# Kernel optimization log

Hardware: AMD Instinct MI355X
Metric: run time of the kernel (lower is better)

The kernel has to match this reference:

```python
import jax, jax.numpy as jnp
import numpy as np
from jax import lax

NUM_BLOCK_X, NUM_BLOCK_Y = 6, 6
NUM_BLOCKS = NUM_BLOCK_X * NUM_BLOCK_Y  # 36


def build_grid_adjacency(nx_, ny_):
    # Mirrors PathFinder128Net.build_grid_adjacency exactly (same edge order).
    src, dst = [], []
    for i in range(nx_):
        for j in range(ny_):
            for dx, dy in [(-1, 0), (0, -1), (0, 1), (1, 0)]:
                x, y = i + dx, j + dy
                if 0 <= x < nx_ and 0 <= y < ny_:
                    src.append(j * nx_ + i)   # block_coord_to_block_id(i, j)
                    dst.append(y * nx_ + x)   # block_coord_to_block_id(x, y)
    return np.asarray(src, np.int32), np.asarray(dst, np.int32)


def setup_inputs() -> dict:
    key = jax.random.key(0)
    ks = jax.random.split(key, 12)
    B = 64
    x = jax.random.normal(ks[0], (B, 1, 128, 128), jnp.float32)
    W = 0.05  # conv init scale
    F = 0.02  # fc init scale
    src, dst = build_grid_adjacency(NUM_BLOCK_X, NUM_BLOCK_Y)  # 120 edges
    n_edges = src.shape[0]
    return {
        "x": x,
        "w1": jax.random.normal(ks[1], (32, 1, 5, 5), jnp.float32) * W,
        "b1": jnp.zeros((32,), jnp.float32),
        "w2": jax.random.normal(ks[2], (32, 32, 5, 5), jnp.float32) * W,
        "b2": jnp.zeros((32,), jnp.float32),
        "w3": jax.random.normal(ks[3], (64, 32, 5, 5), jnp.float32) * W,
        "b3": jnp.zeros((64,), jnp.float32),
        "w4": jax.random.normal(ks[4], (64, 64, 5, 5), jnp.float32) * W,
        "b4": jnp.zeros((64,), jnp.float32),
        "w_ed1": jax.random.normal(ks[5], (1600, 256), jnp.float32) * F,
        "b_ed1": jnp.zeros((256,), jnp.float32),
        "w_ed2": jax.random.normal(ks[6], (256, n_edges), jnp.float32) * F,
        "b_ed2": jnp.zeros((n_edges,), jnp.float32),
        "w_ep1": jax.random.normal(ks[7], (1600, 256), jnp.float32) * F,
        "b_ep1": jnp.zeros((256,), jnp.float32),
        "w_ep2": jax.random.normal(ks[8], (256, NUM_BLOCKS), jnp.float32) * F,
        "b_ep2": jnp.zeros((NUM_BLOCKS,), jnp.float32),
        "edge_src": jnp.asarray(src),
        "edge_dst": jnp.asarray(dst),
    }


def _conv(h, w, b):
    # torch Conv2d, kernel 5, stride 1, no padding, NO activation in between
    h = lax.conv_general_dilated(h, w, (1, 1), "VALID",
                                 dimension_numbers=("NCHW", "OIHW", "NCHW"))
    return h + b[None, :, None, None]


def _pool4(h):
    return lax.reduce_window(h, -jnp.inf, lax.max, (1, 1, 4, 4), (1, 1, 4, 4), "VALID")


def reference(x, w1, b1, w2, b2, w3, b3, w4, b4,
              w_ed1, b_ed1, w_ed2, b_ed2, w_ep1, b_ep1, w_ep2, b_ep2,
              edge_src, edge_dst):
    B = x.shape[0]
    h = _pool4(_conv(_conv(x, w1, b1), w2, b2))          # [B,32,30,30]
    h = _pool4(_conv(_conv(h, w3, b3), w4, b4))          # [B,64,5,5]
    emb = h.reshape(B, -1)                               # [B,1600]

    # edge / endpoint heads: Linear -> ReLU -> Linear -> Sigmoid
    E = jax.nn.sigmoid(jax.nn.relu(emb @ w_ed1 + b_ed1) @ w_ed2 + b_ed2)  # [B,120]
    P = jax.nn.sigmoid(jax.nn.relu(emb @ w_ep1 + b_ep1) @ w_ep2 + b_ep2)  # [B,36]

    # build_paths_recursive with DAMP provenance: symbols are (src,dst) 2-tuples.
    # extend_path maps ((a,b),(b,c)) -> (b,c), i.e. new symbols are already the
    # existing edge set, so the fixpoint terminates after the first iteration
    # (len(merged.symbols) == len(old.symbols)) and is_endpoint is applied to the
    # ORIGINAL connected distribution. A path symbol (u,v) survives is_endpoint
    # conjoined with endpoint evidence at both ends (DAMP conj = product):
    final = E * P[:, edge_src] * P[:, edge_dst]          # [B,120]

    # paths.get_probabilities()[:, 0] -> probability of the first symbol, which
    # is adjacency[0] = (0, 6) for the 6x6 grid.
    return final[:, 0]
```

## Files before the change

kernel.cpp:

```cpp
#include <hip/hip_runtime.h>
#include <math.h>

typedef __attribute__((ext_vector_type(8))) short bf16x8;
typedef __attribute__((ext_vector_type(4))) float f32x4;
typedef unsigned short ushort_t;

#define WS_W12   0
#define WS_B12   2592
#define WS_WMF   2624
#define WS_B34   (2624 + 165888)
#define WS_WMF12 (WS_B34 + 64)
#define WS_P1    (WS_WMF12 + 2560)
#define WS_EMB   (WS_P1 + 64*30*30*32)
#define WS_LOG   (WS_EMB + 102400)
#define WS_WPART WS_P1
#define WS_BPART (WS_P1 + 8*165888)

#define PLST 1880

__device__ __forceinline__ unsigned short f2bf(float f) {
    unsigned u = __float_as_uint(f);
    u += 0x7FFF + ((u >> 16) & 1);
    return (unsigned short)(u >> 16);
}

__global__ __launch_bounds__(128) void k_prep12(
    const float* __restrict__ w1, const float* __restrict__ b1,
    const float* __restrict__ w2, const float* __restrict__ b2,
    float* __restrict__ W12, float* __restrict__ B12)
{
    __shared__ float sW2[800];
    __shared__ float sW1[800];
    int oc = blockIdx.x;
    int t  = threadIdx.x;
    for (int i = t; i < 800; i += 128) {
        sW2[i] = w2[oc * 800 + i];
        sW1[i] = w1[i];
    }
    __syncthreads();
    if (t < 81) {
        int u = t / 9, v = t % 9;
        float acc[4] = {0.f, 0.f, 0.f, 0.f};
        #pragma unroll
        for (int e = 0; e < 25; ++e) {
            int ey = e / 5, ex = e % 5;
            int du = u - ey, dv = v - ex;
            if ((unsigned)du <= 4u && (unsigned)dv <= 4u) {
                int ep = du * 5 + dv;
                for (int mc = 0; mc < 32; ++mc)
                    acc[e & 3] = fmaf(sW2[mc * 25 + e], sW1[mc * 25 + ep],
                                      acc[e & 3]);
            }
        }
        W12[t * 32 + oc] = (acc[0] + acc[1]) + (acc[2] + acc[3]);
    }
    if (t < 32) {
        float ws = 0.f;
        #pragma unroll
        for (int e = 0; e < 25; ++e) ws += sW2[t * 25 + e];
        float p = b1[t] * ws;
        #pragma unroll
        for (int off = 16; off; off >>= 1) p += __shfl_down(p, off, 64);
        if (t == 0) B12[oc] = p + b2[oc];
    }
}

__global__ __launch_bounds__(256) void k_prep34p(
    const float* __restrict__ w3, const float* __restrict__ b3,
    const float* __restrict__ w4,
    float* __restrict__ Wpart, float* __restrict__ Bpart)
{
    __shared__ float sW3c[800];
    int icg = blockIdx.x >> 3;
    int mcc = blockIdx.x & 7;
    int t   = threadIdx.x;
    int oc  = t & 63;
    int icl = t >> 6;
    int ic  = icg * 4 + icl;

    for (int i = t; i < 800; i += 256) {
        int mcl = i / 100, r = i % 100;
        sW3c[i] = w3[(mcc * 8 + mcl) * 800 + icg * 100 + r];
    }
    __syncthreads();

    float acc[81];
    #pragma unroll
    for (int u = 0; u < 81; ++u) acc[u] = 0.f;
    float bacc = 0.f;

    for (int mcl = 0; mcl < 8; ++mcl) {
        int mc = mcc * 8 + mcl;
        float w4r[25];
        #pragma unroll
        for (int e = 0; e < 25; ++e) w4r[e] = w4[oc * 1600 + mc * 25 + e];
        const float* w3r = &sW3c[(mcl * 4 + icl) * 25];
        #pragma unroll
        for (int e2 = 0; e2 < 25; ++e2) {
            int ey = e2 / 5, ex = e2 % 5;
            #pragma unroll
            for (int e1 = 0; e1 < 25; ++e1) {
                int u = (ey + e1 / 5) * 9 + (ex + e1 % 5);
                acc[u] = fmaf(w4r[e2], w3r[e1], acc[u]);
            }
        }
        if (icl == 0) {
            float ws = 0.f;
            #pragma unroll
            for (int e = 0; e < 25; ++e) ws += w4r[e];
            bacc = fmaf(b3[mc], ws, bacc);
        }
    }

    for (int uv = 0; uv < 81; ++uv)
        Wpart[((mcc * 32 + ic) * 81 + uv) * 64 + oc] = acc[uv];
    if (icl == 0) Bpart[mcc * 64 + oc] = bacc;
}

__global__ __launch_bounds__(256) void k_prep34s(
    const float* __restrict__ Wpart, const float* __restrict__ Bpart,
    const float* __restrict__ b4, const float* __restrict__ W12,
    ushort_t* __restrict__ Wmf, float* __restrict__ B34,
    ushort_t* __restrict__ Wmf12)
{
    int bid = blockIdx.x;
    int t   = threadIdx.x;
    int i   = bid * 256 + t;
    if (i < 165888) {
        float s = 0.f;
        #pragma unroll
        for (int c = 0; c < 8; ++c) s += Wpart[c * 165888 + i];
        int oc = i & 63, r = i >> 6;
        int ic = r / 81, uv = r % 81;
        int idx = (uv * 16 + (oc >> 4) * 4 + (ic >> 3)) * 128
                + (oc & 15) * 8 + (ic & 7);
        Wmf[idx] = f2bf(s);
    }
    if (bid == 648 && t < 64) {
        int oc = t;
        float s = b4[oc];
        #pragma unroll
        for (int c = 0; c < 8; ++c) s += Bpart[c * 64 + oc];
        B34[oc] = s;
    }
    if (bid >= 649) {
        int i2 = (bid - 649) * 256 + t;
        int e   = i2 & 7;
        int n   = (i2 >> 3) & 15;
        int kc  = (i2 >> 7) & 3;
        int so  = i2 >> 9;
        int s   = so >> 1, och = so & 1;
        int ky  = 2 * s + (kc >> 1);
        int kx  = 8 * (kc & 1) + e;
        float v = (ky <= 8 && kx <= 8) ? W12[(ky * 9 + kx) * 32 + och * 16 + n]
                                       : 0.f;
        Wmf12[i2] = f2bf(v);
    }
}

__global__ __launch_bounds__(256) void k_conv12m(
    const float* __restrict__ x, const ushort_t* __restrict__ Wmf12,
    const float* __restrict__ B12, ushort_t* __restrict__ P1bf)
{
    __shared__ ushort_t sX[8 * PLST];

    int b  = blockIdx.x / 30;
    int py = blockIdx.x % 30;
    int t  = threadIdx.x;

    if (t < 221) {
        int rowL = t / 17, qg = t % 17;
        int absrow = 4 * py + rowL;
        if (absrow > 127) absrow = 127;
        const float* xr = x + (b * 128 + absrow) * 128;
        int c0 = qg * 8;
        float fs[16];
        #pragma unroll
        for (int q4 = 0; q4 < 4; ++q4) {
            int c = c0 + 4 * q4;
            float4 f;
            if (c <= 124) f = *(const float4*)(xr + c);
            else { f.x = 0.f; f.y = 0.f; f.z = 0.f; f.w = 0.f; }
            fs[4 * q4 + 0] = f.x; fs[4 * q4 + 1] = f.y;
            fs[4 * q4 + 2] = f.z; fs[4 * q4 + 3] = f.w;
        }
        unsigned d[8];
        #pragma unroll
        for (int j = 0; j < 8; ++j)
            d[j] = (unsigned)f2bf(fs[2 * j]) |
                   ((unsigned)f2bf(fs[2 * j + 1]) << 16);
        int eoff = rowL * 144 + c0;
        #pragma unroll
        for (int p = 0; p < 8; ++p) {
            uint4 wv;
            int k = p >> 1;
            if ((p & 1) == 0) {
                wv.x = d[k]; wv.y = d[k + 1]; wv.z = d[k + 2]; wv.w = d[k + 3];
            } else {
                wv.x = (d[k] >> 16)     | (d[k + 1] << 16);
                wv.y = (d[k + 1] >> 16) | (d[k + 2] << 16);
                wv.z = (d[k + 2] >> 16) | (d[k + 3] << 16);
                wv.w = (d[k + 3] >> 16) | (d[k + 4] << 16);
            }
            *(uint4*)(sX + p * PLST + eoff) = wv;
        }
    }

    int l   = t & 63;
    int wv_ = t >> 6;
    int m16 = l & 15;
    int kc  = l >> 4;

    bf16x8 Bf[5][2];
    {
        const ushort_t* wb = Wmf12 + kc * 128 + m16 * 8;
        #pragma unroll
        for (int s = 0; s < 5; ++s)
            #pragma unroll
            for (int och = 0; och < 2; ++och)
                Bf[s][och] = *(const bf16x8*)(wb + (s * 2 + och) * 512);
    }
    float bias0 = B12[m16];
    float bias1 = B12[16 + m16];
    __syncthreads();

    int baseC = (m16 & 7) * PLST + (kc >> 1) * 144
              + 8 * (m16 >> 3) + 8 * (kc & 1);

    #pragma unroll
    for (int xi = 0; xi < 2; ++xi) {
        int xt = wv_ * 2 + xi;
        const ushort_t* ap = sX + baseC + xt * 16;
        float pm0 = -INFINITY, pm1 = -INFINITY;
        #pragma unroll
        for (int y = 0; y < 4; ++y) {
            f32x4 a0 = {0.f, 0.f, 0.f, 0.f}, a1 = a0;
            #pragma unroll
            for (int s = 0; s < 5; ++s) {
                bf16x8 av = *(const bf16x8*)(ap + (y + 2 * s) * 144);
                a0 = __builtin_amdgcn_mfma_f32_16x16x32_bf16(av, Bf[s][0], a0, 0, 0, 0);
                a1 = __builtin_amdgcn_mfma_f32_16x16x32_bf16(av, Bf[s][1], a1, 0, 0, 0);
            }
            pm0 = fmaxf(pm0, fmaxf(fmaxf(a0[0], a0[1]), fmaxf(a0[2], a0[3])));
            pm1 = fmaxf(pm1, fmaxf(fmaxf(a1[0], a1[1]), fmaxf(a1[2], a1[3])));
        }
        int px = xt * 4 + (l >> 4);
        if (px < 30) {
            int ob = ((b * 30 + py) * 30 + px) * 32 + m16;
            P1bf[ob]      = f2bf(pm0 + bias0);
            P1bf[ob + 16] = f2bf(pm1 + bias1);
        }
    }
}

__global__ __launch_bounds__(320) void k_conv34m(
    const ushort_t* __restrict__ P1bf, const ushort_t* __restrict__ Wmf,
    const float* __restrict__ B34, float* __restrict__ emb)
{
    __shared__ ushort_t sA[28 * 960];

    int b  = blockIdx.x >> 2;
    int nt = blockIdx.x & 3;
    int t  = threadIdx.x;

    const uint4* gsrc = (const uint4*)(P1bf + b * 28800);
    for (int i = t; i < 3360; i += 320)
        ((uint4*)sA)[i] = gsrc[i];
    __syncthreads();

    int w  = t >> 6;
    int l  = t & 63;
    int m16 = l & 15;
    int kc  = l >> 4;
    int iy = m16 >> 2, ix = m16 & 3;

    int baseU = (w * 4 + iy) * 960 + ix * 32 + kc * 8;

    f32x4 acc0 = {0.f,0.f,0.f,0.f}, acc1 = acc0, acc2 = acc0,
          acc3 = acc0, acc4 = acc0;

    const ushort_t* wp = Wmf + (nt * 4 + kc) * 128 + m16 * 8;

    bf16x8 bcur = *(const bf16x8*)wp;
    int tap = 0;
    for (int ky = 0; ky < 9; ++ky) {
        int rowU = baseU + ky * 960;
        #pragma unroll
        for (int kx = 0; kx < 9; ++kx) {
            bf16x8 bnext = *(const bf16x8*)(wp + (tap + 1) * 2048);
            const ushort_t* ap = sA + rowU + kx * 32;
            bf16x8 a0 = *(const bf16x8*)(ap);
            bf16x8 a1 = *(const bf16x8*)(ap + 128);
            bf16x8 a2 = *(const bf16x8*)(ap + 256);
            bf16x8 a3 = *(const bf16x8*)(ap + 384);
            bf16x8 a4 = *(const bf16x8*)(ap + 512);
            acc0 = __builtin_amdgcn_mfma_f32_16x16x32_bf16(a0, bcur, acc0, 0, 0, 0);
            acc1 = __builtin_amdgcn_mfma_f32_16x16x32_bf16(a1, bcur, acc1, 0, 0, 0);
            acc2 = __builtin_amdgcn_mfma_f32_16x16x32_bf16(a2, bcur, acc2, 0, 0, 0);
            acc3 = __builtin_amdgcn_mfma_f32_16x16x32_bf16(a3, bcur, acc3, 0, 0, 0);
            acc4 = __builtin_amdgcn_mfma_f32_16x16x32_bf16(a4, bcur, acc4, 0, 0, 0);
            bcur = bnext;
            ++tap;
        }
    }

    float bias = B34[nt * 16 + m16];
    #pragma unroll
    for (int q = 0; q < 5; ++q) {
        f32x4 a = (q == 0) ? acc0 : (q == 1) ? acc1 : (q == 2) ? acc2
                : (q == 3) ? acc3 : acc4;
        float mv = fmaxf(fmaxf(a[0], a[1]), fmaxf(a[2], a[3]));
        mv = fmaxf(mv, __shfl_xor(mv, 16, 64));
        mv = fmaxf(mv, __shfl_xor(mv, 32, 64));
        if (l < 16) {
            int oc = nt * 16 + l;
            emb[b * 1600 + oc * 25 + w * 5 + q] = mv + bias;
        }
    }
}

__global__ __launch_bounds__(512) void k_fc(
    const float* __restrict__ emb,
    const float* __restrict__ w_ed1, const float* __restrict__ b_ed1,
    const float* __restrict__ w_ed2, const float* __restrict__ b_ed2,
    const float* __restrict__ w_ep1, const float* __restrict__ b_ep1,
    const float* __restrict__ w_ep2, const float* __restrict__ b_ep2,
    const int* __restrict__ esrc, const int* __restrict__ edst,
    float* __restrict__ logits)
{
    __shared__ float se[1600];
    __shared__ float sh[2][256];
    __shared__ float sred[2][4];

    int head = blockIdx.x >> 6;
    int b    = blockIdx.x & 63;
    int t    = threadIdx.x;
    int j    = t & 255;
    int kh   = t >> 8;

    {
        const float4* src = (const float4*)(emb + b * 1600);
        for (int i = t; i < 400; i += 512) ((float4*)se)[i] = src[i];
    }
    __syncthreads();

    const float* W1 = head ? w_ep1 : w_ed1;
    float a0 = 0.f, a1 = 0.f, a2 = 0.f, a3 = 0.f;
    int k0 = kh * 800;
    #pragma unroll 8
    for (int k = k0; k < k0 + 800; k += 4) {
        a0 = fmaf(se[k + 0], W1[(k + 0) * 256 + j], a0);
        a1 = fmaf(se[k + 1], W1[(k + 1) * 256 + j], a1);
        a2 = fmaf(se[k + 2], W1[(k + 2) * 256 + j], a2);
        a3 = fmaf(se[k + 3], W1[(k + 3) * 256 + j], a3);
    }
    sh[kh][j] = (a0 + a1) + (a2 + a3);
    __syncthreads();

    int c0 = esrc[0], c1 = edst[0];
    if (t < 256) {
        float bias1 = head ? b_ep1[j] : b_ed1[j];
        float h = fmaxf(bias1 + sh[0][j] + sh[1][j], 0.f);
        if (head == 0) {
            float p = h * w_ed2[j * 120];
            #pragma unroll
            for (int off = 32; off; off >>= 1) p += __shfl_down(p, off, 64);
            if ((t & 63) == 0) sred[0][t >> 6] = p;
        } else {
            float p0 = h * w_ep2[j * 36 + c0];
            float p1 = h * w_ep2[j * 36 + c1];
            #pragma unroll
            for (int off = 32; off; off >>= 1) {
                p0 += __shfl_down(p0, off, 64);
                p1 += __shfl_down(p1, off, 64);
            }
            if ((t & 63) == 0) {
                sred[0][t >> 6] = p0;
                sred[1][t >> 6] = p1;
            }
        }
    }
    __syncthreads();
    if (t == 0) {
        float s0 = (sred[0][0] + sred[0][1]) + (sred[0][2] + sred[0][3]);
        if (head == 0) {
            logits[b * 3 + 0] = s0 + b_ed2[0];
        } else {
            float s1 = (sred[1][0] + sred[1][1]) + (sred[1][2] + sred[1][3]);
            logits[b * 3 + 1] = s0 + b_ep2[c0];
            logits[b * 3 + 2] = s1 + b_ep2[c1];
        }
    }
}

__global__ __launch_bounds__(64) void k_final(
    const float* __restrict__ logits, float* __restrict__ out)
{
    int b = threadIdx.x;
    if (b < 64) {
        float e  = logits[b * 3 + 0];
        float p0 = logits[b * 3 + 1];
        float p1 = logits[b * 3 + 2];
        out[b] = (1.f / (1.f + expf(-e))) *
                 (1.f / (1.f + expf(-p0))) *
                 (1.f / (1.f + expf(-p1)));
    }
}

extern "C" void kernel_launch(void* const* d_in, const int* in_sizes, int n_in,
                              void* d_out, int out_size, void* d_ws, size_t ws_size,
                              hipStream_t stream)
{
    const float* x     = (const float*)d_in[0];
    const float* w1    = (const float*)d_in[1];
    const float* b1    = (const float*)d_in[2];
    const float* w2    = (const float*)d_in[3];
    const float* b2    = (const float*)d_in[4];
    const float* w3    = (const float*)d_in[5];
    const float* b3    = (const float*)d_in[6];
    const float* w4    = (const float*)d_in[7];
    const float* b4    = (const float*)d_in[8];
    const float* w_ed1 = (const float*)d_in[9];
    const float* b_ed1 = (const float*)d_in[10];
    const float* w_ed2 = (const float*)d_in[11];
    const float* b_ed2 = (const float*)d_in[12];
    const float* w_ep1 = (const float*)d_in[13];
    const float* b_ep1 = (const float*)d_in[14];
    const float* w_ep2 = (const float*)d_in[15];
    const float* b_ep2 = (const float*)d_in[16];
    const int*   esrc  = (const int*)d_in[17];
    const int*   edst  = (const int*)d_in[18];

    float* ws  = (float*)d_ws;
    float* out = (float*)d_out;

    ushort_t* Wmf   = (ushort_t*)(ws + WS_WMF);
    ushort_t* Wmf12 = (ushort_t*)(ws + WS_WMF12);
    ushort_t* P1bf  = (ushort_t*)(ws + WS_P1);

    k_prep12<<<32, 128, 0, stream>>>(w1, b1, w2, b2, ws + WS_W12, ws + WS_B12);
    k_prep34p<<<64, 256, 0, stream>>>(w3, b3, w4, ws + WS_WPART, ws + WS_BPART);
    k_prep34s<<<669, 256, 0, stream>>>(ws + WS_WPART, ws + WS_BPART, b4,
                                       ws + WS_W12, Wmf, ws + WS_B34, Wmf12);
    k_conv12m<<<64 * 30, 256, 0, stream>>>(x, Wmf12, ws + WS_B12, P1bf);
    k_conv34m<<<256, 320, 0, stream>>>(P1bf, Wmf, ws + WS_B34, ws + WS_EMB);
    k_fc<<<128, 512, 0, stream>>>(ws + WS_EMB, w_ed1, b_ed1, w_ed2, b_ed2,
                                  w_ep1, b_ep1, w_ep2, b_ep2, esrc, edst,
                                  ws + WS_LOG);
    k_final<<<1, 64, 0, stream>>>(ws + WS_LOG, out);
}
```

Before: 88.69 us.

## Merge prep kernels, fuse FC heads with final sigmoid, preload conv tiles into registers

Merges the conv1/2 weight-prep kernel with the conv3/4 partial-prep kernel and writes the packed conv12 MFMA weights directly from shared memory. The FC heads and the final sigmoid product become one kernel that handles two batch rows per block, so each weight load is reused for two samples. Both conv kernels now preload their input rows from LDS into register arrays before the MFMA loops, and launch-bounds occupancy hints are added. This cuts two launches and redundant LDS reads, at the cost of higher register pressure and fewer FC blocks (32) to hide memory latency.

```diff
diff --git a/kernel.cpp b/kernel.cpp
--- a/kernel.cpp
+++ b/kernel.cpp
@@ -5,18 +5,14 @@
 typedef __attribute__((ext_vector_type(4))) float f32x4;
 typedef unsigned short ushort_t;
 
-#define WS_W12   0
 #define WS_B12   2592
 #define WS_WMF   2624
 #define WS_B34   (2624 + 165888)
 #define WS_WMF12 (WS_B34 + 64)
 #define WS_P1    (WS_WMF12 + 2560)
 #define WS_EMB   (WS_P1 + 64*30*30*32)
-#define WS_LOG   (WS_EMB + 102400)
 #define WS_WPART WS_P1
 #define WS_BPART (WS_P1 + 8*165888)
-
-#define PLST 1880
 
 __device__ __forceinline__ unsigned short f2bf(float f) {
     unsigned u = __float_as_uint(f);
@@ -24,108 +20,119 @@
     return (unsigned short)(u >> 16);
 }
 
-__global__ __launch_bounds__(128) void k_prep12(
+__global__ __launch_bounds__(256) void k_prepA(
     const float* __restrict__ w1, const float* __restrict__ b1,
     const float* __restrict__ w2, const float* __restrict__ b2,
-    float* __restrict__ W12, float* __restrict__ B12)
-{
-    __shared__ float sW2[800];
-    __shared__ float sW1[800];
-    int oc = blockIdx.x;
-    int t  = threadIdx.x;
-    for (int i = t; i < 800; i += 128) {
-        sW2[i] = w2[oc * 800 + i];
-        sW1[i] = w1[i];
-    }
-    __syncthreads();
-    if (t < 81) {
-        int u = t / 9, v = t % 9;
-        float acc[4] = {0.f, 0.f, 0.f, 0.f};
-        #pragma unroll
-        for (int e = 0; e < 25; ++e) {
-            int ey = e / 5, ex = e % 5;
-            int du = u - ey, dv = v - ex;
-            if ((unsigned)du <= 4u && (unsigned)dv <= 4u) {
-                int ep = du * 5 + dv;
-                for (int mc = 0; mc < 32; ++mc)
-                    acc[e & 3] = fmaf(sW2[mc * 25 + e], sW1[mc * 25 + ep],
-                                      acc[e & 3]);
-            }
-        }
-        W12[t * 32 + oc] = (acc[0] + acc[1]) + (acc[2] + acc[3]);
-    }
-    if (t < 32) {
-        float ws = 0.f;
-        #pragma unroll
-        for (int e = 0; e < 25; ++e) ws += sW2[t * 25 + e];
-        float p = b1[t] * ws;
-        #pragma unroll
-        for (int off = 16; off; off >>= 1) p += __shfl_down(p, off, 64);
-        if (t == 0) B12[oc] = p + b2[oc];
-    }
-}
-
-__global__ __launch_bounds__(256) void k_prep34p(
     const float* __restrict__ w3, const float* __restrict__ b3,
     const float* __restrict__ w4,
+    float* __restrict__ B12, ushort_t* __restrict__ Wmf12,
     float* __restrict__ Wpart, float* __restrict__ Bpart)
 {
-    __shared__ float sW3c[800];
-    int icg = blockIdx.x >> 3;
-    int mcc = blockIdx.x & 7;
-    int t   = threadIdx.x;
-    int oc  = t & 63;
-    int icl = t >> 6;
-    int ic  = icg * 4 + icl;
-
-    for (int i = t; i < 800; i += 256) {
-        int mcl = i / 100, r = i % 100;
-        sW3c[i] = w3[(mcc * 8 + mcl) * 800 + icg * 100 + r];
-    }
-    __syncthreads();
-
-    float acc[81];
-    #pragma unroll
-    for (int u = 0; u < 81; ++u) acc[u] = 0.f;
-    float bacc = 0.f;
-
-    for (int mcl = 0; mcl < 8; ++mcl) {
-        int mc = mcc * 8 + mcl;
-        float w4r[25];
-        #pragma unroll
-        for (int e = 0; e < 25; ++e) w4r[e] = w4[oc * 1600 + mc * 25 + e];
-        const float* w3r = &sW3c[(mcl * 4 + icl) * 25];
-        #pragma unroll
-        for (int e2 = 0; e2 < 25; ++e2) {
-            int ey = e2 / 5, ex = e2 % 5;
-            #pragma unroll
-            for (int e1 = 0; e1 < 25; ++e1) {
-                int u = (ey + e1 / 5) * 9 + (ex + e1 % 5);
-                acc[u] = fmaf(w4r[e2], w3r[e1], acc[u]);
+    __shared__ float smem[1681];
+    int t = threadIdx.x;
+
+    if (blockIdx.x < 32) {
+        float* sW2  = smem;
+        float* sW1  = smem + 800;
+        float* sW12 = smem + 1600;
+        int oc = blockIdx.x;
+        for (int i = t; i < 800; i += 256) {
+            sW2[i] = w2[oc * 800 + i];
+            sW1[i] = w1[i];
+        }
+        __syncthreads();
+        if (t < 81) {
+            int u = t / 9, v = t % 9;
+            float acc[4] = {0.f, 0.f, 0.f, 0.f};
+            #pragma unroll
+            for (int e = 0; e < 25; ++e) {
+                int ey = e / 5, ex = e % 5;
+                int du = u - ey, dv = v - ex;
+                if ((unsigned)du <= 4u && (unsigned)dv <= 4u) {
+                    int ep = du * 5 + dv;
+                    for (int mc = 0; mc < 32; ++mc)
+                        acc[e & 3] = fmaf(sW2[mc * 25 + e], sW1[mc * 25 + ep],
+                                          acc[e & 3]);
+                }
             }
-        }
-        if (icl == 0) {
+            sW12[t] = (acc[0] + acc[1]) + (acc[2] + acc[3]);
+        }
+        if (t < 32) {
             float ws = 0.f;
             #pragma unroll
-            for (int e = 0; e < 25; ++e) ws += w4r[e];
-            bacc = fmaf(b3[mc], ws, bacc);
-        }
-    }
-
-    for (int uv = 0; uv < 81; ++uv)
-        Wpart[((mcc * 32 + ic) * 81 + uv) * 64 + oc] = acc[uv];
-    if (icl == 0) Bpart[mcc * 64 + oc] = bacc;
+            for (int e = 0; e < 25; ++e) ws += sW2[t * 25 + e];
+            float p = b1[t] * ws;
+            #pragma unroll
+            for (int off = 16; off; off >>= 1) p += __shfl_down(p, off, 64);
+            if (t == 0) B12[oc] = p + b2[oc];
+        }
+        __syncthreads();
+        if (t < 160) {
+            int s  = t >> 5;
+            int kc = (t >> 3) & 3;
+            int e  = t & 7;
+            int ky = 2 * s + (kc >> 1);
+            int kx = 8 * (kc & 1) + e;
+            float v = (ky <= 8 && kx <= 8) ? sW12[ky * 9 + kx] : 0.f;
+            int so = s * 2 + (oc >> 4);
+            int i2 = (so << 9) | (kc << 7) | ((oc & 15) << 3) | e;
+            Wmf12[i2] = f2bf(v);
+        }
+    } else {
+        float* sW3c = smem;
+        int bid = blockIdx.x - 32;
+        int icg = bid >> 3;
+        int mcc = bid & 7;
+        int oc  = t & 63;
+        int icl = t >> 6;
+        int ic  = icg * 4 + icl;
+
+        for (int i = t; i < 800; i += 256) {
+            int mcl = i / 100, r = i % 100;
+            sW3c[i] = w3[(mcc * 8 + mcl) * 800 + icg * 100 + r];
+        }
+        __syncthreads();
+
+        float acc[81];
+        #pragma unroll
+        for (int u = 0; u < 81; ++u) acc[u] = 0.f;
+        float bacc = 0.f;
+
+        for (int mcl = 0; mcl < 8; ++mcl) {
+            int mc = mcc * 8 + mcl;
+            float w4r[25];
+            #pragma unroll
+            for (int e = 0; e < 25; ++e) w4r[e] = w4[oc * 1600 + mc * 25 + e];
+            const float* w3r = &sW3c[(mcl * 4 + icl) * 25];
+            #pragma unroll
+            for (int e2 = 0; e2 < 25; ++e2) {
+                int ey = e2 / 5, ex = e2 % 5;
+                #pragma unroll
+                for (int e1 = 0; e1 < 25; ++e1) {
+                    int u = (ey + e1 / 5) * 9 + (ex + e1 % 5);
+                    acc[u] = fmaf(w4r[e2], w3r[e1], acc[u]);
+                }
+            }
+            if (icl == 0) {
+                float ws = 0.f;
+                #pragma unroll
+                for (int e = 0; e < 25; ++e) ws += w4r[e];
+                bacc = fmaf(b3[mc], ws, bacc);
+            }
+        }
+
+        for (int uv = 0; uv < 81; ++uv)
+            Wpart[((mcc * 32 + ic) * 81 + uv) * 64 + oc] = acc[uv];
+        if (icl == 0) Bpart[mcc * 64 + oc] = bacc;
+    }
 }
 
 __global__ __launch_bounds__(256) void k_prep34s(
     const float* __restrict__ Wpart, const float* __restrict__ Bpart,
-    const float* __restrict__ b4, const float* __restrict__ W12,
-    ushort_t* __restrict__ Wmf, float* __restrict__ B34,
-    ushort_t* __restrict__ Wmf12)
-{
-    int bid = blockIdx.x;
-    int t   = threadIdx.x;
-    int i   = bid * 256 + t;
+    const float* __restrict__ b4,
+    ushort_t* __restrict__ Wmf, float* __restrict__ B34)
+{
+    int i = blockIdx.x * 256 + threadIdx.x;
     if (i < 165888) {
         float s = 0.f;
         #pragma unroll
@@ -136,33 +143,20 @@
                 + (oc & 15) * 8 + (ic & 7);
         Wmf[idx] = f2bf(s);
     }
-    if (bid == 648 && t < 64) {
-        int oc = t;
+    if (blockIdx.x == 648 && threadIdx.x < 64) {
+        int oc = threadIdx.x;
         float s = b4[oc];
         #pragma unroll
         for (int c = 0; c < 8; ++c) s += Bpart[c * 64 + oc];
         B34[oc] = s;
     }
-    if (bid >= 649) {
-        int i2 = (bid - 649) * 256 + t;
-        int e   = i2 & 7;
-        int n   = (i2 >> 3) & 15;
-        int kc  = (i2 >> 7) & 3;
-        int so  = i2 >> 9;
-        int s   = so >> 1, och = so & 1;
-        int ky  = 2 * s + (kc >> 1);
-        int kx  = 8 * (kc & 1) + e;
-        float v = (ky <= 8 && kx <= 8) ? W12[(ky * 9 + kx) * 32 + och * 16 + n]
-                                       : 0.f;
-        Wmf12[i2] = f2bf(v);
-    }
-}
-
-__global__ __launch_bounds__(256) void k_conv12m(
+}
+
+__global__ __launch_bounds__(256, 2) void k_conv12m(
     const float* __restrict__ x, const ushort_t* __restrict__ Wmf12,
     const float* __restrict__ B12, ushort_t* __restrict__ P1bf)
 {
-    __shared__ ushort_t sX[8 * PLST];
+    __shared__ ushort_t sX[8 * 1880];
 
     int b  = blockIdx.x / 30;
     int py = blockIdx.x % 30;
@@ -202,7 +196,7 @@
                 wv.z = (d[k + 2] >> 16) | (d[k + 3] << 16);
                 wv.w = (d[k + 3] >> 16) | (d[k + 4] << 16);
             }
-            *(uint4*)(sX + p * PLST + eoff) = wv;
+            *(uint4*)(sX + p * 1880 + eoff) = wv;
         }
     }
 
@@ -224,22 +218,26 @@
     float bias1 = B12[16 + m16];
     __syncthreads();
 
-    int baseC = (m16 & 7) * PLST + (kc >> 1) * 144
+    int baseC = (m16 & 7) * 1880 + (kc >> 1) * 144
               + 8 * (m16 >> 3) + 8 * (kc & 1);
 
     #pragma unroll
     for (int xi = 0; xi < 2; ++xi) {
         int xt = wv_ * 2 + xi;
         const ushort_t* ap = sX + baseC + xt * 16;
+        bf16x8 T[12];
+        #pragma unroll
+        for (int r = 0; r < 12; ++r)
+            T[r] = *(const bf16x8*)(ap + r * 144);
+
         float pm0 = -INFINITY, pm1 = -INFINITY;
         #pragma unroll
         for (int y = 0; y < 4; ++y) {
             f32x4 a0 = {0.f, 0.f, 0.f, 0.f}, a1 = a0;
             #pragma unroll
             for (int s = 0; s < 5; ++s) {
-                bf16x8 av = *(const bf16x8*)(ap + (y + 2 * s) * 144);
-                a0 = __builtin_amdgcn_mfma_f32_16x16x32_bf16(av, Bf[s][0], a0, 0, 0, 0);
-                a1 = __builtin_amdgcn_mfma_f32_16x16x32_bf16(av, Bf[s][1], a1, 0, 0, 0);
+                a0 = __builtin_amdgcn_mfma_f32_16x16x32_bf16(T[y + 2 * s], Bf[s][0], a0, 0, 0, 0);
+                a1 = __builtin_amdgcn_mfma_f32_16x16x32_bf16(T[y + 2 * s], Bf[s][1], a1, 0, 0, 0);
             }
             pm0 = fmaxf(pm0, fmaxf(fmaxf(a0[0], a0[1]), fmaxf(a0[2], a0[3])));
             pm1 = fmaxf(pm1, fmaxf(fmaxf(a1[0], a1[1]), fmaxf(a1[2], a1[3])));
@@ -253,7 +251,7 @@
     }
 }
 
-__global__ __launch_bounds__(320) void k_conv34m(
+__global__ __launch_bounds__(320, 1) void k_conv34m(
     const ushort_t* __restrict__ P1bf, const ushort_t* __restrict__ Wmf,
     const float* __restrict__ B34, float* __restrict__ emb)
 {
@@ -274,31 +272,28 @@
     int kc  = l >> 4;
     int iy = m16 >> 2, ix = m16 & 3;
 
-    int baseU = (w * 4 + iy) * 960 + ix * 32 + kc * 8;
-
     f32x4 acc0 = {0.f,0.f,0.f,0.f}, acc1 = acc0, acc2 = acc0,
           acc3 = acc0, acc4 = acc0;
 
     const ushort_t* wp = Wmf + (nt * 4 + kc) * 128 + m16 * 8;
-
     bf16x8 bcur = *(const bf16x8*)wp;
     int tap = 0;
+
     for (int ky = 0; ky < 9; ++ky) {
-        int rowU = baseU + ky * 960;
+        const ushort_t* rp = sA + (w * 4 + iy + ky) * 960 + ix * 32 + kc * 8;
+        bf16x8 T[25];
+        #pragma unroll
+        for (int cx = 0; cx < 25; ++cx)
+            T[cx] = *(const bf16x8*)(rp + cx * 32);
+
         #pragma unroll
         for (int kx = 0; kx < 9; ++kx) {
             bf16x8 bnext = *(const bf16x8*)(wp + (tap + 1) * 2048);
-            const ushort_t* ap = sA + rowU + kx * 32;
-            bf16x8 a0 = *(const bf16x8*)(ap);
-            bf16x8 a1 = *(const bf16x8*)(ap + 128);
-            bf16x8 a2 = *(const bf16x8*)(ap + 256);
-            bf16x8 a3 = *(const bf16x8*)(ap + 384);
-            bf16x8 a4 = *(const bf16x8*)(ap + 512);
-            acc0 = __builtin_amdgcn_mfma_f32_16x16x32_bf16(a0, bcur, acc0, 0, 0, 0);
-            acc1 = __builtin_amdgcn_mfma_f32_16x16x32_bf16(a1, bcur, acc1, 0, 0, 0);
-            acc2 = __builtin_amdgcn_mfma_f32_16x16x32_bf16(a2, bcur, acc2, 0, 0, 0);
-            acc3 = __builtin_amdgcn_mfma_f32_16x16x32_bf16(a3, bcur, acc3, 0, 0, 0);
-            acc4 = __builtin_amdgcn_mfma_f32_16x16x32_bf16(a4, bcur, acc4, 0, 0, 0);
+            acc0 = __builtin_amdgcn_mfma_f32_16x16x32_bf16(T[kx],      bcur, acc0, 0, 0, 0);
+            acc1 = __builtin_amdgcn_mfma_f32_16x16x32_bf16(T[kx + 4],  bcur, acc1, 0, 0, 0);
+            acc2 = __builtin_amdgcn_mfma_f32_16x16x32_bf16(T[kx + 8],  bcur, acc2, 0, 0, 0);
+            acc3 = __builtin_amdgcn_mfma_f32_16x16x32_bf16(T[kx + 12], bcur, acc3, 0, 0, 0);
+            acc4 = __builtin_amdgcn_mfma_f32_16x16x32_bf16(T[kx + 16], bcur, acc4, 0, 0, 0);
             bcur = bnext;
             ++tap;
         }
@@ -319,91 +314,76 @@
     }
 }
 
-__global__ __launch_bounds__(512) void k_fc(
+__global__ __launch_bounds__(1024) void k_fcall(
     const float* __restrict__ emb,
     const float* __restrict__ w_ed1, const float* __restrict__ b_ed1,
     const float* __restrict__ w_ed2, const float* __restrict__ b_ed2,
     const float* __restrict__ w_ep1, const float* __restrict__ b_ep1,
     const float* __restrict__ w_ep2, const float* __restrict__ b_ep2,
     const int* __restrict__ esrc, const int* __restrict__ edst,
-    float* __restrict__ logits)
-{
-    __shared__ float se[1600];
-    __shared__ float sh[2][256];
-    __shared__ float sred[2][4];
-
-    int head = blockIdx.x >> 6;
-    int b    = blockIdx.x & 63;
-    int t    = threadIdx.x;
-    int j    = t & 255;
-    int kh   = t >> 8;
-
-    {
-        const float4* src = (const float4*)(emb + b * 1600);
-        for (int i = t; i < 400; i += 512) ((float4*)se)[i] = src[i];
-    }
-    __syncthreads();
-
-    const float* W1 = head ? w_ep1 : w_ed1;
-    float a0 = 0.f, a1 = 0.f, a2 = 0.f, a3 = 0.f;
+    float* __restrict__ out)
+{
+    __shared__ float se[2][1600];
+    __shared__ float sh[2][512];
+    __shared__ float sp[6];
+
+    int b0 = blockIdx.x * 2;
+    int t  = threadIdx.x;
+
+    for (int i = t; i < 800; i += 1024) {
+        int bb = i / 400, q = i % 400;
+        ((float4*)se[bb])[q] = ((const float4*)(emb + (b0 + bb) * 1600))[q];
+    }
+    __syncthreads();
+
+    int j  = t & 511;
+    int kh = t >> 9;
+    int jj = j & 255;
+    const float* W1 = (j < 256) ? w_ed1 : w_ep1;
+    float a00 = 0.f, a01 = 0.f, a10 = 0.f, a11 = 0.f;
     int k0 = kh * 800;
-    #pragma unroll 8
-    for (int k = k0; k < k0 + 800; k += 4) {
-        a0 = fmaf(se[k + 0], W1[(k + 0) * 256 + j], a0);
-        a1 = fmaf(se[k + 1], W1[(k + 1) * 256 + j], a1);
-        a2 = fmaf(se[k + 2], W1[(k + 2) * 256 + j], a2);
-        a3 = fmaf(se[k + 3], W1[(k + 3) * 256 + j], a3);
-    }
-    sh[kh][j] = (a0 + a1) + (a2 + a3);
+    #pragma unroll 4
+    for (int k = k0; k < k0 + 800; k += 2) {
+        float w0 = W1[(k + 0) * 256 + jj];
+        float w1 = W1[(k + 1) * 256 + jj];
+        a00 = fmaf(se[0][k + 0], w0, a00);
+        a01 = fmaf(se[0][k + 1], w1, a01);
+        a10 = fmaf(se[1][k + 0], w0, a10);
+        a11 = fmaf(se[1][k + 1], w1, a11);
+    }
+    if (kh == 0) { sh[0][j] = a00 + a01; sh[1][j] = a10 + a11; }
+    __syncthreads();
+    if (kh == 1) { sh[0][j] += a00 + a01; sh[1][j] += a10 + a11; }
     __syncthreads();
 
     int c0 = esrc[0], c1 = edst[0];
-    if (t < 256) {
-        float bias1 = head ? b_ep1[j] : b_ed1[j];
-        float h = fmaxf(bias1 + sh[0][j] + sh[1][j], 0.f);
-        if (head == 0) {
-            float p = h * w_ed2[j * 120];
-            #pragma unroll
-            for (int off = 32; off; off >>= 1) p += __shfl_down(p, off, 64);
-            if ((t & 63) == 0) sred[0][t >> 6] = p;
-        } else {
-            float p0 = h * w_ep2[j * 36 + c0];
-            float p1 = h * w_ep2[j * 36 + c1];
-            #pragma unroll
-            for (int off = 32; off; off >>= 1) {
-                p0 += __shfl_down(p0, off, 64);
-                p1 += __shfl_down(p1, off, 64);
-            }
-            if ((t & 63) == 0) {
-                sred[0][t >> 6] = p0;
-                sred[1][t >> 6] = p1;
-            }
-        }
-    }
-    __syncthreads();
-    if (t == 0) {
-        float s0 = (sred[0][0] + sred[0][1]) + (sred[0][2] + sred[0][3]);
-        if (head == 0) {
-            logits[b * 3 + 0] = s0 + b_ed2[0];
-        } else {
-            float s1 = (sred[1][0] + sred[1][1]) + (sred[1][2] + sred[1][3]);
-            logits[b * 3 + 1] = s0 + b_ep2[c0];
-            logits[b * 3 + 2] = s1 + b_ep2[c1];
-        }
-    }
-}
-
-__global__ __launch_bounds__(64) void k_final(
-    const float* __restrict__ logits, float* __restrict__ out)
-{
-    int b = threadIdx.x;
-    if (b < 64) {
-        float e  = logits[b * 3 + 0];
-        float p0 = logits[b * 3 + 1];
-        float p1 = logits[b * 3 + 2];
-        out[b] = (1.f / (1.f + expf(-e))) *
-                 (1.f / (1.f + expf(-p0))) *
-                 (1.f / (1.f + expf(-p1)));
+    if (t < 384) {
+        int lane = t & 63;
+        int q6   = t >> 6;
+        int q    = q6 % 3;
+        int bb   = q6 / 3;
+        int head = q > 0;
+        float acc = 0.f;
+        for (int jl = lane; jl < 256; jl += 64) {
+            float bias1 = head ? b_ep1[jl] : b_ed1[jl];
+            float h = fmaxf(sh[bb][head * 256 + jl] + bias1, 0.f);
+            float wgt = (q == 0) ? w_ed2[jl * 120]
+                      : (q == 1) ? w_ep2[jl * 36 + c0]
+                                 : w_ep2[jl * 36 + c1];
+            acc = fmaf(h, wgt, acc);
+        }
+        #pragma unroll
+        for (int off = 32; off; off >>= 1) acc += __shfl_down(acc, off, 64);
+        if (lane == 0) sp[q6] = acc;
+    }
+    __syncthreads();
+    if (t < 2) {
+        float le = sp[t * 3 + 0] + b_ed2[0];
+        float l0 = sp[t * 3 + 1] + b_ep2[c0];
+        float l1 = sp[t * 3 + 2] + b_ep2[c1];
+        out[b0 + t] = (1.f / (1.f + expf(-le))) *
+                      (1.f / (1.f + expf(-l0))) *
+                      (1.f / (1.f + expf(-l1)));
     }
 }
 
@@ -438,14 +418,14 @@
     ushort_t* Wmf12 = (ushort_t*)(ws + WS_WMF12);
     ushort_t* P1bf  = (ushort_t*)(ws + WS_P1);
 
-    k_prep12<<<32, 128, 0, stream>>>(w1, b1, w2, b2, ws + WS_W12, ws + WS_B12);
-    k_prep34p<<<64, 256, 0, stream>>>(w3, b3, w4, ws + WS_WPART, ws + WS_BPART);
-    k_prep34s<<<669, 256, 0, stream>>>(ws + WS_WPART, ws + WS_BPART, b4,
-                                       ws + WS_W12, Wmf, ws + WS_B34, Wmf12);
+    k_prepA<<<96, 256, 0, stream>>>(w1, b1, w2, b2, w3, b3, w4,
+                                    ws + WS_B12, Wmf12,
+                                    ws + WS_WPART, ws + WS_BPART);
+    k_prep34s<<<649, 256, 0, stream>>>(ws + WS_WPART, ws + WS_BPART, b4,
+                                       Wmf, ws + WS_B34);
     k_conv12m<<<64 * 30, 256, 0, stream>>>(x, Wmf12, ws + WS_B12, P1bf);
     k_conv34m<<<256, 320, 0, stream>>>(P1bf, Wmf, ws + WS_B34, ws + WS_EMB);
-    k_fc<<<128, 512, 0, stream>>>(ws + WS_EMB, w_ed1, b_ed1, w_ed2, b_ed2,
-                                  w_ep1, b_ep1, w_ep2, b_ep2, esrc, edst,
-                                  ws + WS_LOG);
-    k_final<<<1, 64, 0, stream>>>(ws + WS_LOG, out);
-}
+    k_fcall<<<32, 1024, 0, stream>>>(ws + WS_EMB, w_ed1, b_ed1, w_ed2, b_ed2,
+                                     w_ep1, b_ep1, w_ep2, b_ep2, esrc, edst,
+                                     out);
+}
```

New measurement: 100.4 us. 1.13x slower.

## Merge weight-prep kernels and cache conv input rows in registers

Applied to the files above, without the earlier changes.

Merges the conv1/2 weight-fold kernel with the conv3/4 partial fold into one launch and writes the MFMA-layout Wmf12 directly from shared memory, which removes one kernel launch and the W12 global round trip. Both conv kernels now load each row's input fragments into register arrays once and reuse them across the overlapping taps, which cuts redundant LDS reads. Launch bounds gain occupancy hints. The larger register arrays (25 bf16x8 in conv34) could cause spills or lower occupancy.

```diff
diff --git a/kernel.cpp b/kernel.cpp
--- a/kernel.cpp
+++ b/kernel.cpp
@@ -5,7 +5,6 @@
 typedef __attribute__((ext_vector_type(4))) float f32x4;
 typedef unsigned short ushort_t;
 
-#define WS_W12   0
 #define WS_B12   2592
 #define WS_WMF   2624
 #define WS_B34   (2624 + 165888)
@@ -16,116 +15,125 @@
 #define WS_WPART WS_P1
 #define WS_BPART (WS_P1 + 8*165888)
 
-#define PLST 1880
-
 __device__ __forceinline__ unsigned short f2bf(float f) {
     unsigned u = __float_as_uint(f);
     u += 0x7FFF + ((u >> 16) & 1);
     return (unsigned short)(u >> 16);
 }
 
-__global__ __launch_bounds__(128) void k_prep12(
+__global__ __launch_bounds__(256) void k_prepA(
     const float* __restrict__ w1, const float* __restrict__ b1,
     const float* __restrict__ w2, const float* __restrict__ b2,
-    float* __restrict__ W12, float* __restrict__ B12)
-{
-    __shared__ float sW2[800];
-    __shared__ float sW1[800];
-    int oc = blockIdx.x;
-    int t  = threadIdx.x;
-    for (int i = t; i < 800; i += 128) {
-        sW2[i] = w2[oc * 800 + i];
-        sW1[i] = w1[i];
-    }
-    __syncthreads();
-    if (t < 81) {
-        int u = t / 9, v = t % 9;
-        float acc[4] = {0.f, 0.f, 0.f, 0.f};
-        #pragma unroll
-        for (int e = 0; e < 25; ++e) {
-            int ey = e / 5, ex = e % 5;
-            int du = u - ey, dv = v - ex;
-            if ((unsigned)du <= 4u && (unsigned)dv <= 4u) {
-                int ep = du * 5 + dv;
-                for (int mc = 0; mc < 32; ++mc)
-                    acc[e & 3] = fmaf(sW2[mc * 25 + e], sW1[mc * 25 + ep],
-                                      acc[e & 3]);
-            }
-        }
-        W12[t * 32 + oc] = (acc[0] + acc[1]) + (acc[2] + acc[3]);
-    }
-    if (t < 32) {
-        float ws = 0.f;
-        #pragma unroll
-        for (int e = 0; e < 25; ++e) ws += sW2[t * 25 + e];
-        float p = b1[t] * ws;
-        #pragma unroll
-        for (int off = 16; off; off >>= 1) p += __shfl_down(p, off, 64);
-        if (t == 0) B12[oc] = p + b2[oc];
-    }
-}
-
-__global__ __launch_bounds__(256) void k_prep34p(
     const float* __restrict__ w3, const float* __restrict__ b3,
     const float* __restrict__ w4,
+    float* __restrict__ B12, ushort_t* __restrict__ Wmf12,
     float* __restrict__ Wpart, float* __restrict__ Bpart)
 {
-    __shared__ float sW3c[800];
-    int icg = blockIdx.x >> 3;
-    int mcc = blockIdx.x & 7;
-    int t   = threadIdx.x;
-    int oc  = t & 63;
-    int icl = t >> 6;
-    int ic  = icg * 4 + icl;
-
-    for (int i = t; i < 800; i += 256) {
-        int mcl = i / 100, r = i % 100;
-        sW3c[i] = w3[(mcc * 8 + mcl) * 800 + icg * 100 + r];
-    }
-    __syncthreads();
-
-    float acc[81];
-    #pragma unroll
-    for (int u = 0; u < 81; ++u) acc[u] = 0.f;
-    float bacc = 0.f;
-
-    for (int mcl = 0; mcl < 8; ++mcl) {
-        int mc = mcc * 8 + mcl;
-        float w4r[25];
-        #pragma unroll
-        for (int e = 0; e < 25; ++e) w4r[e] = w4[oc * 1600 + mc * 25 + e];
-        const float* w3r = &sW3c[(mcl * 4 + icl) * 25];
-        #pragma unroll
-        for (int e2 = 0; e2 < 25; ++e2) {
-            int ey = e2 / 5, ex = e2 % 5;
-            #pragma unroll
-            for (int e1 = 0; e1 < 25; ++e1) {
-                int u = (ey + e1 / 5) * 9 + (ex + e1 % 5);
-                acc[u] = fmaf(w4r[e2], w3r[e1], acc[u]);
-            }
-        }
-        if (icl == 0) {
+    __shared__ float smem[1681];
+    int t = threadIdx.x;
+
+    if (blockIdx.x < 32) {
+        float* sW2  = smem;
+        float* sW1  = smem + 800;
+        float* sW12 = smem + 1600;
+        int oc = blockIdx.x;
+        for (int i = t; i < 800; i += 256) {
+            sW2[i] = w2[oc * 800 + i];
+            sW1[i] = w1[i];
+        }
+        __syncthreads();
+        if (t < 81) {
+            int u = t / 9, v = t % 9;
+            float acc[4] = {0.f, 0.f, 0.f, 0.f};
+            #pragma unroll
+            for (int e = 0; e < 25; ++e) {
+                int ey = e / 5, ex = e % 5;
+                int du = u - ey, dv = v - ex;
+                if ((unsigned)du <= 4u && (unsigned)dv <= 4u) {
+                    int ep = du * 5 + dv;
+                    for (int mc = 0; mc < 32; ++mc)
+                        acc[e & 3] = fmaf(sW2[mc * 25 + e], sW1[mc * 25 + ep],
+                                          acc[e & 3]);
+                }
+            }
+            sW12[t] = (acc[0] + acc[1]) + (acc[2] + acc[3]);
+        }
+        if (t < 32) {
             float ws = 0.f;
             #pragma unroll
-            for (int e = 0; e < 25; ++e) ws += w4r[e];
-            bacc = fmaf(b3[mc], ws, bacc);
-        }
-    }
-
-    for (int uv = 0; uv < 81; ++uv)
-        Wpart[((mcc * 32 + ic) * 81 + uv) * 64 + oc] = acc[uv];
-    if (icl == 0) Bpart[mcc * 64 + oc] = bacc;
+            for (int e = 0; e < 25; ++e) ws += sW2[t * 25 + e];
+            float p = b1[t] * ws;
+            #pragma unroll
+            for (int off = 16; off; off >>= 1) p += __shfl_down(p, off, 64);
+            if (t == 0) B12[oc] = p + b2[oc];
+        }
+        __syncthreads();
+        if (t < 160) {
+            int s  = t >> 5;
+            int kc = (t >> 3) & 3;
+            int e  = t & 7;
+            int ky = 2 * s + (kc >> 1);
+            int kx = 8 * (kc & 1) + e;
+            float v = (ky <= 8 && kx <= 8) ? sW12[ky * 9 + kx] : 0.f;
+            int so = s * 2 + (oc >> 4);
+            int i2 = (so << 9) | (kc << 7) | ((oc & 15) << 3) | e;
+            Wmf12[i2] = f2bf(v);
+        }
+    } else {
+        float* sW3c = smem;
+        int bid = blockIdx.x - 32;
+        int icg = bid >> 3;
+        int mcc = bid & 7;
+        int oc  = t & 63;
+        int icl = t >> 6;
+        int ic  = icg * 4 + icl;
+
+        for (int i = t; i < 800; i += 256) {
+            int mcl = i / 100, r = i % 100;
+            sW3c[i] = w3[(mcc * 8 + mcl) * 800 + icg * 100 + r];
+        }
+        __syncthreads();
+
+        float acc[81];
+        #pragma unroll
+        for (int u = 0; u < 81; ++u) acc[u] = 0.f;
+        float bacc = 0.f;
+
+        for (int mcl = 0; mcl < 8; ++mcl) {
+            int mc = mcc * 8 + mcl;
+            float w4r[25];
+            #pragma unroll
+            for (int e = 0; e < 25; ++e) w4r[e] = w4[oc * 1600 + mc * 25 + e];
+            const float* w3r = &sW3c[(mcl * 4 + icl) * 25];
+            #pragma unroll
+            for (int e2 = 0; e2 < 25; ++e2) {
+                int ey = e2 / 5, ex = e2 % 5;
+                #pragma unroll
+                for (int e1 = 0; e1 < 25; ++e1) {
+                    int u = (ey + e1 / 5) * 9 + (ex + e1 % 5);
+                    acc[u] = fmaf(w4r[e2], w3r[e1], acc[u]);
+                }
+            }
+            if (icl == 0) {
+                float ws = 0.f;
+                #pragma unroll
+                for (int e = 0; e < 25; ++e) ws += w4r[e];
+                bacc = fmaf(b3[mc], ws, bacc);
+            }
+        }
+
+        for (int uv = 0; uv < 81; ++uv)
+            Wpart[((mcc * 32 + ic) * 81 + uv) * 64 + oc] = acc[uv];
+        if (icl == 0) Bpart[mcc * 64 + oc] = bacc;
+    }
 }
 
 __global__ __launch_bounds__(256) void k_prep34s(
     const float* __restrict__ Wpart, const float* __restrict__ Bpart,
-    const float* __restrict__ b4, const float* __restrict__ W12,
-    ushort_t* __restrict__ Wmf, float* __restrict__ B34,
-    ushort_t* __restrict__ Wmf12)
-{
-    int bid = blockIdx.x;
-    int t   = threadIdx.x;
-    int i   = bid * 256 + t;
+    const float* __restrict__ b4,
+    ushort_t* __restrict__ Wmf, float* __restrict__ B34)
+{
+    int i = blockIdx.x * 256 + threadIdx.x;
     if (i < 165888) {
         float s = 0.f;
         #pragma unroll
@@ -136,33 +144,20 @@
                 + (oc & 15) * 8 + (ic & 7);
         Wmf[idx] = f2bf(s);
     }
-    if (bid == 648 && t < 64) {
-        int oc = t;
+    if (blockIdx.x == 648 && threadIdx.x < 64) {
+        int oc = threadIdx.x;
         float s = b4[oc];
         #pragma unroll
         for (int c = 0; c < 8; ++c) s += Bpart[c * 64 + oc];
         B34[oc] = s;
     }
-    if (bid >= 649) {
-        int i2 = (bid - 649) * 256 + t;
-        int e   = i2 & 7;
-        int n   = (i2 >> 3) & 15;
-        int kc  = (i2 >> 7) & 3;
-        int so  = i2 >> 9;
-        int s   = so >> 1, och = so & 1;
-        int ky  = 2 * s + (kc >> 1);
-        int kx  = 8 * (kc & 1) + e;
-        float v = (ky <= 8 && kx <= 8) ? W12[(ky * 9 + kx) * 32 + och * 16 + n]
-                                       : 0.f;
-        Wmf12[i2] = f2bf(v);
-    }
-}
-
-__global__ __launch_bounds__(256) void k_conv12m(
+}
+
+__global__ __launch_bounds__(256, 2) void k_conv12m(
     const float* __restrict__ x, const ushort_t* __restrict__ Wmf12,
     const float* __restrict__ B12, ushort_t* __restrict__ P1bf)
 {
-    __shared__ ushort_t sX[8 * PLST];
+    __shared__ ushort_t sX[8 * 1880];
 
     int b  = blockIdx.x / 30;
     int py = blockIdx.x % 30;
@@ -202,7 +197,7 @@
                 wv.z = (d[k + 2] >> 16) | (d[k + 3] << 16);
                 wv.w = (d[k + 3] >> 16) | (d[k + 4] << 16);
             }
-            *(uint4*)(sX + p * PLST + eoff) = wv;
+            *(uint4*)(sX + p * 1880 + eoff) = wv;
         }
     }
 
@@ -224,22 +219,26 @@
     float bias1 = B12[16 + m16];
     __syncthreads();
 
-    int baseC = (m16 & 7) * PLST + (kc >> 1) * 144
+    int baseC = (m16 & 7) * 1880 + (kc >> 1) * 144
               + 8 * (m16 >> 3) + 8 * (kc & 1);
 
     #pragma unroll
     for (int xi = 0; xi < 2; ++xi) {
         int xt = wv_ * 2 + xi;
         const ushort_t* ap = sX + baseC + xt * 16;
+        bf16x8 T[12];
+        #pragma unroll
+        for (int r = 0; r < 12; ++r)
+            T[r] = *(const bf16x8*)(ap + r * 144);
+
         float pm0 = -INFINITY, pm1 = -INFINITY;
         #pragma unroll
         for (int y = 0; y < 4; ++y) {
             f32x4 a0 = {0.f, 0.f, 0.f, 0.f}, a1 = a0;
             #pragma unroll
             for (int s = 0; s < 5; ++s) {
-                bf16x8 av = *(const bf16x8*)(ap + (y + 2 * s) * 144);
-                a0 = __builtin_amdgcn_mfma_f32_16x16x32_bf16(av, Bf[s][0], a0, 0, 0, 0);
-                a1 = __builtin_amdgcn_mfma_f32_16x16x32_bf16(av, Bf[s][1], a1, 0, 0, 0);
+                a0 = __builtin_amdgcn_mfma_f32_16x16x32_bf16(T[y + 2 * s], Bf[s][0], a0, 0, 0, 0);
+                a1 = __builtin_amdgcn_mfma_f32_16x16x32_bf16(T[y + 2 * s], Bf[s][1], a1, 0, 0, 0);
             }
             pm0 = fmaxf(pm0, fmaxf(fmaxf(a0[0], a0[1]), fmaxf(a0[2], a0[3])));
             pm1 = fmaxf(pm1, fmaxf(fmaxf(a1[0], a1[1]), fmaxf(a1[2], a1[3])));
@@ -253,7 +252,7 @@
     }
 }
 
-__global__ __launch_bounds__(320) void k_conv34m(
+__global__ __launch_bounds__(320, 1) void k_conv34m(
     const ushort_t* __restrict__ P1bf, const ushort_t* __restrict__ Wmf,
     const float* __restrict__ B34, float* __restrict__ emb)
 {
@@ -274,31 +273,28 @@
     int kc  = l >> 4;
     int iy = m16 >> 2, ix = m16 & 3;
 
-    int baseU = (w * 4 + iy) * 960 + ix * 32 + kc * 8;
-
     f32x4 acc0 = {0.f,0.f,0.f,0.f}, acc1 = acc0, acc2 = acc0,
           acc3 = acc0, acc4 = acc0;
 
     const ushort_t* wp = Wmf + (nt * 4 + kc) * 128 + m16 * 8;
-
     bf16x8 bcur = *(const bf16x8*)wp;
     int tap = 0;
+
     for (int ky = 0; ky < 9; ++ky) {
-        int rowU = baseU + ky * 960;
+        const ushort_t* rp = sA + (w * 4 + iy + ky) * 960 + ix * 32 + kc * 8;
+        bf16x8 T[25];
+        #pragma unroll
+        for (int cx = 0; cx < 25; ++cx)
+            T[cx] = *(const bf16x8*)(rp + cx * 32);
+
         #pragma unroll
         for (int kx = 0; kx < 9; ++kx) {
             bf16x8 bnext = *(const bf16x8*)(wp + (tap + 1) * 2048);
-            const ushort_t* ap = sA + rowU + kx * 32;
-            bf16x8 a0 = *(const bf16x8*)(ap);
-            bf16x8 a1 = *(const bf16x8*)(ap + 128);
-            bf16x8 a2 = *(const bf16x8*)(ap + 256);
-            bf16x8 a3 = *(const bf16x8*)(ap + 384);
-            bf16x8 a4 = *(const bf16x8*)(ap + 512);
-            acc0 = __builtin_amdgcn_mfma_f32_16x16x32_bf16(a0, bcur, acc0, 0, 0, 0);
-            acc1 = __builtin_amdgcn_mfma_f32_16x16x32_bf16(a1, bcur, acc1, 0, 0, 0);
-            acc2 = __builtin_amdgcn_mfma_f32_16x16x32_bf16(a2, bcur, acc2, 0, 0, 0);
-            acc3 = __builtin_amdgcn_mfma_f32_16x16x32_bf16(a3, bcur, acc3, 0, 0, 0);
-            acc4 = __builtin_amdgcn_mfma_f32_16x16x32_bf16(a4, bcur, acc4, 0, 0, 0);
+            acc0 = __builtin_amdgcn_mfma_f32_16x16x32_bf16(T[kx],      bcur, acc0, 0, 0, 0);
+            acc1 = __builtin_amdgcn_mfma_f32_16x16x32_bf16(T[kx + 4],  bcur, acc1, 0, 0, 0);
+            acc2 = __builtin_amdgcn_mfma_f32_16x16x32_bf16(T[kx + 8],  bcur, acc2, 0, 0, 0);
+            acc3 = __builtin_amdgcn_mfma_f32_16x16x32_bf16(T[kx + 12], bcur, acc3, 0, 0, 0);
+            acc4 = __builtin_amdgcn_mfma_f32_16x16x32_bf16(T[kx + 16], bcur, acc4, 0, 0, 0);
             bcur = bnext;
             ++tap;
         }
@@ -438,10 +434,11 @@
     ushort_t* Wmf12 = (ushort_t*)(ws + WS_WMF12);
     ushort_t* P1bf  = (ushort_t*)(ws + WS_P1);
 
-    k_prep12<<<32, 128, 0, stream>>>(w1, b1, w2, b2, ws + WS_W12, ws + WS_B12);
-    k_prep34p<<<64, 256, 0, stream>>>(w3, b3, w4, ws + WS_WPART, ws + WS_BPART);
-    k_prep34s<<<669, 256, 0, stream>>>(ws + WS_WPART, ws + WS_BPART, b4,
-                                       ws + WS_W12, Wmf, ws + WS_B34, Wmf12);
+    k_prepA<<<96, 256, 0, stream>>>(w1, b1, w2, b2, w3, b3, w4,
+                                    ws + WS_B12, Wmf12,
+                                    ws + WS_WPART, ws + WS_BPART);
+    k_prep34s<<<649, 256, 0, stream>>>(ws + WS_WPART, ws + WS_BPART, b4,
+                                       Wmf, ws + WS_B34);
     k_conv12m<<<64 * 30, 256, 0, stream>>>(x, Wmf12, ws + WS_B12, P1bf);
     k_conv34m<<<256, 320, 0, stream>>>(P1bf, Wmf, ws + WS_B34, ws + WS_EMB);
     k_fc<<<128, 512, 0, stream>>>(ws + WS_EMB, w_ed1, b_ed1, w_ed2, b_ed2,
```

After: 76.80 us. 13.4% less time.
